# Kernel tuning notes

Measured on AMD Instinct MI355X. Metric: run time of the kernel, lower is better.

The kernel has to match this reference:

```python
import jax, jax.numpy as jnp
import numpy as np

K = 9        # kNN neighbors (ViG default kernel_size=9)
EPS = 1e-5   # BatchNorm eps


def _bn2d(x, gamma, beta):
    # training-mode BatchNorm2d over (B,H,W) per channel; x: [B,C,H,W]
    mean = jnp.mean(x, axis=(0, 2, 3), keepdims=True)
    var = jnp.var(x, axis=(0, 2, 3), keepdims=True)
    g = gamma.reshape(1, -1, 1, 1)
    b = beta.reshape(1, -1, 1, 1)
    return g * (x - mean) * jax.lax.rsqrt(var + EPS) + b


def setup_inputs() -> dict:
    key = jax.random.key(0)
    B, C, H, W = 8, 96, 56, 56
    oup = 192
    ks = jax.random.split(key, 8)
    sc = 0.05
    return {
        "x": jax.random.normal(ks[0], (B, C, H, W), dtype=jnp.float32),
        "W_fc1": jax.random.normal(ks[1], (C, C), dtype=jnp.float32) * sc,
        "b_fc1": jnp.zeros((C,), jnp.float32),
        "g_bn1": jnp.ones((C,), jnp.float32),
        "be_bn1": jnp.zeros((C,), jnp.float32),
        "W_edge": jax.random.normal(ks[2], (2 * C, 2 * C), dtype=jnp.float32) * sc,
        "b_edge": jnp.zeros((2 * C,), jnp.float32),
        "g_bne": jnp.ones((2 * C,), jnp.float32),
        "be_bne": jnp.zeros((2 * C,), jnp.float32),
        "W_fc2": jax.random.normal(ks[3], (2 * C, C), dtype=jnp.float32) * sc,
        "b_fc2": jnp.zeros((C,), jnp.float32),
        "g_bn2": jnp.ones((C,), jnp.float32),
        "be_bn2": jnp.zeros((C,), jnp.float32),
        "g_sabn": jnp.ones((C,), jnp.float32),
        "be_sabn": jnp.zeros((C,), jnp.float32),
        "W_dw": jax.random.normal(ks[4], (oup, C, 3, 3), dtype=jnp.float32) * sc,
        "b_dw": jnp.zeros((oup,), jnp.float32),
        "g_dwbn": jnp.ones((oup,), jnp.float32),
        "be_dwbn": jnp.zeros((oup,), jnp.float32),
    }


def reference(x, W_fc1, b_fc1, g_bn1, be_bn1, W_edge, b_edge, g_bne, be_bne,
              W_fc2, b_fc2, g_bn2, be_bn2, g_sabn, be_sabn,
              W_dw, b_dw, g_dwbn, be_dwbn):
    B, C, H, W = x.shape
    N = H * W
    shortcut = x

    # --- Grapher.fc1: 1x1 conv + BN ---
    y = jnp.einsum('bchw,cd->bdhw', x, W_fc1) + b_fc1[None, :, None, None]
    y = _bn2d(y, g_bn1, be_bn1)

    # --- dynamic kNN graph over flattened tokens ---
    ft = y.reshape(B, C, N).transpose(0, 2, 1)            # [B,N,C]
    sq = jnp.sum(ft * ft, axis=-1)                        # [B,N]
    dist = sq[:, :, None] - 2.0 * jnp.einsum('bnc,bmc->bnm', ft, ft) + sq[:, None, :]
    _, idx = jax.lax.top_k(-dist, K)                      # [B,N,K] nearest neighbors

    # --- EdgeConv: max_k act(BN(W [x_i, x_j - x_i])) ---
    x_j = jnp.take_along_axis(ft[:, :, None, :], idx[..., None], axis=1)  # [B,N,K,C]
    x_i = ft[:, :, None, :]                               # [B,N,1,C]
    e = jnp.concatenate([jnp.broadcast_to(x_i, x_j.shape), x_j - x_i], axis=-1)  # [B,N,K,2C]
    e = jnp.einsum('bnkc,cd->bnkd', e, W_edge) + b_edge
    m = jnp.mean(e, axis=(0, 1, 2))
    v = jnp.var(e, axis=(0, 1, 2))
    e = g_bne * (e - m) * jax.lax.rsqrt(v + EPS) + be_bne
    e = jax.nn.relu(e)
    g = jnp.max(e, axis=2)                                # [B,N,2C] max-aggregation

    # --- Grapher.fc2: 1x1 conv + BN, residual ---
    g = jnp.einsum('bnc,cd->bnd', g, W_fc2) + b_fc2       # [B,N,C]
    g = g.transpose(0, 2, 1).reshape(B, C, H, W)
    g = _bn2d(g, g_bn2, be_bn2)
    y = g + shortcut

    # --- SAEncoder: BN + ReLU ---
    y = jax.nn.relu(_bn2d(y, g_sabn, be_sabn))

    # --- convdw: 3x3 stride-2 conv + BN + ReLU ---
    y = jax.lax.conv_general_dilated(
        y, W_dw, window_strides=(2, 2), padding=((1, 1), (1, 1)),
        dimension_numbers=('NCHW', 'OIHW', 'NCHW')) + b_dw[None, :, None, None]
    y = jax.nn.relu(_bn2d(y, g_dwbn, be_dwbn))
    return y
```

## Files before the change

### kernel.cpp

```cpp
#include <hip/hip_runtime.h>
#include <math.h>

#define B_   8
#define C_   96
#define C2_  192
#define N_   3136
#define R_   25088
#define OUP_ 192
#define HO_  28
#define NO_  784
#define EPS_ 1e-5f
#define QS2  128
#define CAP3 64

typedef short bf16x8 __attribute__((ext_vector_type(8)));
typedef float f32x4  __attribute__((ext_vector_type(4)));

__device__ __forceinline__ int swz16(int i) { return (i & ~15) | ((i & 15) ^ ((i >> 4) & 7)); }

__global__ __launch_bounds__(512) void k_fc1_d(const float* __restrict__ x,
                                               const float* __restrict__ W1,
                                               const float* __restrict__ b1,
                                               double* __restrict__ yd) {
    __shared__ double Wl[96 * 48];
    int tid = threadIdx.x;
    int rl = tid & 255, h = tid >> 8;
    int dbase = blockIdx.y * 48;
    for (int q = tid; q < 96 * 48; q += 512) {
        int c = q / 48, dd = q % 48;
        Wl[c * 48 + dd] = (double)W1[c * 96 + dbase + dd];
    }
    __syncthreads();
    int r = blockIdx.x * 256 + rl;
    int b = r / N_;
    int n = r - b * N_;
    double acc[24];
#pragma unroll
    for (int i = 0; i < 24; i++) acc[i] = 0.0;
    const float* xp = x + (size_t)b * C_ * N_ + n;
    for (int c = 0; c < 96; ++c) {
        double xv = (double)xp[(size_t)c * N_];
        const double* w = &Wl[c * 48 + h * 24];
#pragma unroll
        for (int i = 0; i < 24; ++i) acc[i] += xv * w[i];
    }
    int d0 = dbase + h * 24;
#pragma unroll
    for (int i = 0; i < 24; i++) {
        int d = d0 + i;
        yd[((size_t)b * C_ + d) * N_ + n] = acc[i] + (double)b1[d];
    }
}

__global__ __launch_bounds__(256) void k_stats_chan_d(const double* __restrict__ src,
                                                      double* __restrict__ partial) {
    int c = blockIdx.x;
    int chunk = blockIdx.y;
    const int SPLIT = 16;
    double s = 0.0, ss = 0.0;
    for (int j = chunk * 256 + threadIdx.x; j < R_; j += SPLIT * 256) {
        int b = j / N_, n = j - b * N_;
        double v = src[((size_t)b * C_ + c) * N_ + n];
        s += v;
        ss += v * v;
    }
    __shared__ double red[8];
    for (int off = 32; off; off >>= 1) {
        s += __shfl_down(s, off, 64);
        ss += __shfl_down(ss, off, 64);
    }
    int lane = threadIdx.x & 63, w = threadIdx.x >> 6;
    if (lane == 0) { red[w * 2] = s; red[w * 2 + 1] = ss; }
    __syncthreads();
    if (threadIdx.x == 0) {
        s = red[0] + red[2] + red[4] + red[6];
        ss = red[1] + red[3] + red[5] + red[7];
        partial[(c * SPLIT + chunk) * 2] = s;
        partial[(c * SPLIT + chunk) * 2 + 1] = ss;
    }
}

__global__ void k_stats_reduce_d(const double* __restrict__ partial, double* __restrict__ stats) {
    int c = blockIdx.x * blockDim.x + threadIdx.x;
    if (c >= 96) return;
    double s = 0.0, ss = 0.0;
    for (int k = 0; k < 16; k++) {
        s += partial[(c * 16 + k) * 2];
        ss += partial[(c * 16 + k) * 2 + 1];
    }
    double m = s / (double)R_;
    double var = ss / (double)R_ - m * m;
    stats[c * 2] = m;
    stats[c * 2 + 1] = 1.0 / sqrt(var + 1e-5);
}

__global__ void k_stats_reduce(const float* __restrict__ partial, float* __restrict__ stats,
                               int Cn, int SPLIT, float invcount) {
    int c = blockIdx.x * blockDim.x + threadIdx.x;
    if (c >= Cn) return;
    float s = 0.f, ss = 0.f;
    for (int k = 0; k < SPLIT; k++) {
        s += partial[(c * SPLIT + k) * 2];
        ss += partial[(c * SPLIT + k) * 2 + 1];
    }
    float m = s * invcount;
    float var = ss * invcount - m * m;
    stats[c * 2] = m;
    stats[c * 2 + 1] = 1.0f / sqrtf(var + EPS_);
}

__global__ __launch_bounds__(256) void k_stats_reduce_g(const float* __restrict__ partial,
                                                        float* __restrict__ stats,
                                                        int Cn, int NB, float invcount) {
    int c = blockIdx.x;
    float s = 0.f, ss = 0.f;
    for (int k = threadIdx.x; k < NB; k += 256) {
        s  += partial[(size_t)k * 2 * Cn + c];
        ss += partial[(size_t)k * 2 * Cn + Cn + c];
    }
    __shared__ float red[8];
    for (int off = 32; off; off >>= 1) {
        s += __shfl_down(s, off, 64);
        ss += __shfl_down(ss, off, 64);
    }
    int lane = threadIdx.x & 63, w = threadIdx.x >> 6;
    if (lane == 0) { red[w * 2] = s; red[w * 2 + 1] = ss; }
    __syncthreads();
    if (threadIdx.x == 0) {
        s = red[0] + red[2] + red[4] + red[6];
        ss = red[1] + red[3] + red[5] + red[7];
        float m = s * invcount;
        float var = ss * invcount - m * m;
        stats[c * 2] = m;
        stats[c * 2 + 1] = 1.0f / sqrtf(var + EPS_);
    }
}

__global__ __launch_bounds__(256) void k_bn1_tr(const double* __restrict__ yd,
                                                const double* __restrict__ stats,
                                                const float* __restrict__ g,
                                                const float* __restrict__ be,
                                                float* __restrict__ ftc,
                                                double* __restrict__ ftp64,
                                                unsigned short* __restrict__ fspH,
                                                double* __restrict__ sq64) {
    __shared__ double tile[64 * 97];
    __shared__ double dsq[64][4];
    int b = blockIdx.y;
    int n0 = blockIdx.x * 64;
    int tid = threadIdx.x;
    int n = tid & 63, w = tid >> 6;
    for (int k = 0; k < 24; ++k) {
        int c = k * 4 + w;
        size_t gi = ((size_t)b * C_ + c) * N_ + n0 + n;
        double m = stats[c * 2], rs = stats[c * 2 + 1];
        double v = (double)g[c] * (yd[gi] - m) * rs + (double)be[c];
        ftc[gi] = (float)v;
        tile[n * 97 + c] = v;
    }
    __syncthreads();
    int p = n, q = w;
    double vals[24];
    double s = 0.0;
    const double* lp = &tile[p * 97 + q * 24];
#pragma unroll
    for (int m2 = 0; m2 < 24; ++m2) { vals[m2] = lp[m2]; s += vals[m2] * vals[m2]; }
    dsq[p][q] = s;
    double* dst = ftp64 + ((size_t)b * N_ + n0 + p) * C_ + q * 24;
#pragma unroll
    for (int m2 = 0; m2 < 24; m2 += 2) *(double2*)&dst[m2] = make_double2(vals[m2], vals[m2 + 1]);
    unsigned* hdst = (unsigned*)(fspH + ((size_t)b * N_ + n0 + p) * QS2);
#pragma unroll
    for (int m2 = 0; m2 < 24; m2 += 2) {
        unsigned u0 = __float_as_uint((float)vals[m2]);
        unsigned u1 = __float_as_uint((float)vals[m2 + 1]);
        unsigned h0 = (u0 + 0x7fffu + ((u0 >> 16) & 1u)) >> 16;
        unsigned h1 = (u1 + 0x7fffu + ((u1 >> 16) & 1u)) >> 16;
        hdst[q * 12 + (m2 >> 1)] = h0 | (h1 << 16);
    }
    __syncthreads();
    if (tid < 64) {
        double tot = dsq[tid][0] + dsq[tid][1] + dsq[tid][2] + dsq[tid][3];
        sq64[(size_t)b * N_ + n0 + tid] = tot;
        float t32 = (float)(-0.5 * tot);
        unsigned u0 = __float_as_uint(t32);
        unsigned h0 = (u0 + 0x7fffu + ((u0 >> 16) & 1u)) >> 16;
        float resid = t32 - __uint_as_float(h0 << 16);
        unsigned u1 = __float_as_uint(resid);
        unsigned h1 = (u1 + 0x7fffu + ((u1 >> 16) & 1u)) >> 16;
        unsigned* hd = (unsigned*)(fspH + ((size_t)b * N_ + n0 + tid) * QS2);
        hd[48] = h0 | (h1 << 16);
#pragma unroll
        for (int k2 = 49; k2 < 64; ++k2) hd[k2] = 0u;
    }
}

__global__ __launch_bounds__(256) void k_dist6(const unsigned short* __restrict__ fspH,
                                               unsigned short* __restrict__ poolC,
                                               unsigned* __restrict__ poolCnt) {
    __shared__ __align__(16) char lds[54016];
    float*          cminF = (float*)(lds + 32768);
    unsigned short* poolL = (unsigned short*)(lds + 45312);
    unsigned*       cntL  = (unsigned*)(lds + 53504);
    float*          t9fL  = (float*)(lds + 53760);

    int b = blockIdx.y;
    int q0 = blockIdx.x * 64;
    int tid = threadIdx.x;
    int w = tid >> 6, l = tid & 63;

    {
        const uint4* src = (const uint4*)(fspH + ((size_t)b * N_ + q0) * QS2);
        uint4* dst = (uint4*)lds;
        for (int i = tid; i < 1024; i += 256) dst[swz16(i)] = src[i];
    }
    __syncthreads();
    bf16x8 Bq[4];
    {
        const unsigned short* Ql = (const unsigned short*)lds;
        int qr = w * 16 + (l & 15);
#pragma unroll
        for (int s = 0; s < 3; ++s) {
            int col = (s * 4 + (l >> 4)) ^ (qr & 7);
            Bq[s] = *(const bf16x8*)&Ql[qr * QS2 + col * 8];
        }
        bf16x8 z = {0, 0, 0, 0, 0, 0, 0, 0};
        if ((l >> 4) == 0) { z[0] = (short)0x3F80; z[1] = (short)0x3F80; }
        Bq[3] = z;
    }
    __syncthreads();

    {
        const uint4* src = (const uint4*)(fspH + (size_t)b * N_ * QS2);
        uint4* dst = (uint4*)lds;
        for (int i = tid; i < 1024; i += 256) dst[swz16(i)] = src[i];
    }
    __syncthreads();

    float thr2r = 1e30f;
    int cur = 0;
    for (int t = 0; t < 98; ++t) {
        int ch = (t < 49) ? t : t - 49;
        int c0 = ch * 64;
        bool pf = (t < 97);
        uint4 st0, st1, st2, st3;
        if (pf) {
            int nch = (t + 1 < 49) ? (t + 1) : (t + 1 - 49);
            const uint4* src = (const uint4*)(fspH + ((size_t)b * N_ + nch * 64) * QS2);
            st0 = src[tid]; st1 = src[tid + 256]; st2 = src[tid + 512]; st3 = src[tid + 768];
        }
        const unsigned short* Bc = (const unsigned short*)(lds + cur * 16384);
        f32x4 acc[4];
#pragma unroll
        for (int ct = 0; ct < 4; ++ct) acc[ct] = (f32x4){0.f, 0.f, 0.f, 0.f};
#pragma unroll
        for (int s = 0; s < 4; ++s) {
#pragma unroll
            for (int ct = 0; ct < 4; ++ct) {
                int cr = ct * 16 + (l & 15);
                int col = (s * 4 + (l >> 4)) ^ (cr & 7);
                bf16x8 Ac = *(const bf16x8*)&Bc[cr * QS2 + col * 8];
                acc[ct] = __builtin_amdgcn_mfma_f32_16x16x32_bf16(Ac, Bq[s], acc[ct], 0, 0, 0);
            }
        }
        if (t < 49) {
            float mx = -1e30f;
#pragma unroll
            for (int ct = 0; ct < 4; ++ct)
#pragma unroll
                for (int j = 0; j < 4; ++j) mx = fmaxf(mx, acc[ct][j]);
            mx = fmaxf(mx, __shfl_xor(mx, 16, 64));
            mx = fmaxf(mx, __shfl_xor(mx, 32, 64));
            if (l < 16) cminF[ch * 64 + w * 16 + l] = -2.f * mx;
        } else {
            int qrow = w * 16 + (l & 15);
#pragma unroll
            for (int ct = 0; ct < 4; ++ct)
#pragma unroll
                for (int j = 0; j < 4; ++j) {
                    if (acc[ct][j] >= thr2r) {
                        unsigned pos = atomicAdd(&cntL[qrow], 1u);
                        if (pos < (unsigned)CAP3)
                            poolL[qrow * CAP3 + pos] = (unsigned short)(c0 + ct * 16 + (l >> 4) * 4 + j);
                    }
                }
        }
        if (t == 48) {
            __syncthreads();
            if (tid < 64) {
                float top[9];
#pragma unroll
                for (int j = 0; j < 9; ++j) top[j] = 1e30f;
                for (int q = 0; q < 49; ++q) {
                    float v = cminF[q * 64 + tid];
                    if (v < top[8]) {
                        top[8] = v;
#pragma unroll
                        for (int j = 8; j >= 1; --j)
                            if (top[j] < top[j - 1]) { float tt = top[j]; top[j] = top[j - 1]; top[j - 1] = tt; }
                    }
                }
                float t9 = top[8] + fabsf(top[8]) * 0.008f + 0.75f;
                t9fL[tid] = -0.5f * t9;
                cntL[tid] = 0u;
            }
            __syncthreads();
            thr2r = t9fL[w * 16 + (l & 15)];
        }
        if (pf) {
            uint4* dst = (uint4*)(lds + (cur ^ 1) * 16384);
            dst[swz16(tid)] = st0;
            dst[swz16(tid + 256)] = st1;
            dst[swz16(tid + 512)] = st2;
            dst[swz16(tid + 768)] = st3;
        }
        __syncthreads();
        cur ^= 1;
    }
    if (tid < 64) {
        unsigned c = cntL[tid];
        poolCnt[(size_t)b * N_ + q0 + tid] = (c > (unsigned)CAP3) ? (unsigned)CAP3 : c;
    }
    {
        unsigned* dst = (unsigned*)(poolC + ((size_t)b * N_ + q0) * CAP3);
        const unsigned* src = (const unsigned*)poolL;
        for (int i = tid; i < 64 * CAP3 / 2; i += 256) dst[i] = src[i];
    }
}

__global__ __launch_bounds__(256) void k_rerank_d(const unsigned short* __restrict__ poolC,
                                                  const unsigned* __restrict__ poolCnt,
                                                  const double* __restrict__ ftp64,
                                                  const double* __restrict__ sq64,
                                                  int* __restrict__ idx) {
    int tid = threadIdx.x;
    int wv = tid >> 6, l = tid & 63;
    int rr = blockIdx.x * 4 + wv;
    int b = rr / N_;
    int cnt = (int)poolCnt[rr];
    if (cnt > CAP3) cnt = CAP3;
    int e = l & 3;
    double qreg[24];
    {
        const double* qb = ftp64 + (size_t)rr * C_ + e * 24;
#pragma unroll
        for (int m = 0; m < 24; ++m) qreg[m] = qb[m];
    }
    double dv[4];
    int jv[4];
#pragma unroll
    for (int gG = 0; gG < 4; ++gG) { dv[gG] = 1e300; jv[gG] = 0x7fffffff; }
#pragma unroll
    for (int gG = 0; gG < 4; ++gG) {
        if (gG * 16 >= cnt) break;
        int ci = gG * 16 + (l >> 2);
        bool valid = ci < cnt;
        int j = valid ? (int)poolC[(size_t)rr * CAP3 + ci] : 0;
        const double* cb = ftp64 + ((size_t)b * N_ + j) * C_ + e * 24;
        double p = 0.0;
#pragma unroll
        for (int m = 0; m < 24; ++m) p += qreg[m] * cb[m];
        p += __shfl_xor(p, 1, 64);
        p += __shfl_xor(p, 2, 64);
        if (valid) {
            dv[gG] = sq64[(size_t)b * N_ + j] - 2.0 * p;
            jv[gG] = j;
        }
    }
#pragma unroll
    for (int r = 0; r < 9; ++r) {
        double dm = dv[0]; int jm = jv[0];
#pragma unroll
        for (int gG = 1; gG < 4; ++gG)
            if (dv[gG] < dm || (dv[gG] == dm && jv[gG] < jm)) { dm = dv[gG]; jm = jv[gG]; }
#pragma unroll
        for (int off = 1; off <= 32; off <<= 1) {
            double od = __shfl_xor(dm, off, 64);
            int oj = __shfl_xor(jm, off, 64);
            if (od < dm || (od == dm && oj < jm)) { dm = od; jm = oj; }
        }
        if (l == 0) idx[(size_t)rr * 9 + r] = jm;
#pragma unroll
        for (int gG = 0; gG < 4; ++gG)
            if (jv[gG] == jm) dv[gG] = 1e300;
    }
}

__global__ __launch_bounds__(512) void k_gemm_uv2(const float* __restrict__ ftc,
                                                  const float* __restrict__ We,
                                                  const float* __restrict__ beb,
                                                  float* __restrict__ u,
                                                  float* __restrict__ v) {
    __shared__ float Wl[2][96 * 48];
    int tid = threadIdx.x;
    int rl = tid & 255, h = tid >> 8;
    int dbase = blockIdx.y * 48;
    for (int q = tid; q < 96 * 48; q += 512) {
        int c = q / 48, dd = q % 48;
        float wb = We[(96 + c) * C2_ + dbase + dd];
        Wl[1][q] = wb;
        Wl[0][q] = We[c * C2_ + dbase + dd] - wb;
    }
    __syncthreads();
    int r = blockIdx.x * 256 + rl;
    int b = r / N_, n = r - b * N_;
    float a0[24], a1[24];
#pragma unroll
    for (int i = 0; i < 24; i++) { a0[i] = 0.f; a1[i] = 0.f; }
    const float* xp = ftc + (size_t)b * C_ * N_ + n;
    for (int c = 0; c < 96; ++c) {
        float xv = xp[(size_t)c * N_];
        const float4* w40 = (const float4*)&Wl[0][c * 48 + h * 24];
        const float4* w41 = (const float4*)&Wl[1][c * 48 + h * 24];
#pragma unroll
        for (int i = 0; i < 6; ++i) {
            float4 w0 = w40[i], w1 = w41[i];
            a0[i * 4 + 0] += xv * w0.x; a0[i * 4 + 1] += xv * w0.y;
            a0[i * 4 + 2] += xv * w0.z; a0[i * 4 + 3] += xv * w0.w;
            a1[i * 4 + 0] += xv * w1.x; a1[i * 4 + 1] += xv * w1.y;
            a1[i * 4 + 2] += xv * w1.z; a1[i * 4 + 3] += xv * w1.w;
        }
    }
    int d0 = dbase + h * 24;
    float* up = u + (size_t)r * C2_ + d0;
    float* vp = v + (size_t)r * C2_ + d0;
#pragma unroll
    for (int i = 0; i < 6; ++i) {
        float4 ou, ov;
        ou.x = a0[i * 4 + 0] + beb[d0 + i * 4 + 0];
        ou.y = a0[i * 4 + 1] + beb[d0 + i * 4 + 1];
        ou.z = a0[i * 4 + 2] + beb[d0 + i * 4 + 2];
        ou.w = a0[i * 4 + 3] + beb[d0 + i * 4 + 3];
        ov.x = a1[i * 4 + 0]; ov.y = a1[i * 4 + 1];
        ov.z = a1[i * 4 + 2]; ov.w = a1[i * 4 + 3];
        ((float4*)up)[i] = ou;
        ((float4*)vp)[i] = ov;
    }
}

__global__ __launch_bounds__(192) void k_bne_stats(const float* __restrict__ u,
                                                   const float* __restrict__ v,
                                                   const int* __restrict__ idx,
                                                   float* __restrict__ partial) {
    int d = threadIdx.x;
    int row0 = blockIdx.x * 32;
    int b = row0 / N_;
    float s = 0.f, ss = 0.f;
    for (int r = 0; r < 32; ++r) {
        int row = row0 + r;
        float ud = u[(size_t)row * C2_ + d];
        const int* ip = idx + (size_t)row * 9;
#pragma unroll
        for (int k = 0; k < 9; k++) {
            int j = ip[k];
            float e = ud + v[((size_t)b * N_ + j) * C2_ + d];
            s += e;
            ss += e * e;
        }
    }
    partial[(size_t)blockIdx.x * 384 + d] = s;
    partial[(size_t)blockIdx.x * 384 + 192 + d] = ss;
}

__global__ __launch_bounds__(192) void k_edge_fc2_st(const float* __restrict__ u,
                                                     const float* __restrict__ v,
                                                     const int* __restrict__ idx,
                                                     const float* __restrict__ statsE,
                                                     const float* __restrict__ ge,
                                                     const float* __restrict__ bee,
                                                     const float* __restrict__ W2,
                                                     const float* __restrict__ b2,
                                                     float* __restrict__ out2,
                                                     float* __restrict__ partialE) {
    __shared__ float gl[16][C2_];
    __shared__ float g2[C_][16];
    int tid = threadIdx.x;
    int row0 = blockIdx.x * 16;
    int b = row0 / N_;
    int n0 = row0 - b * N_;
    {
        int d = tid;
        float m = statsE[d * 2], rs = statsE[d * 2 + 1];
        float ga = ge[d], bb = bee[d];
        for (int r = 0; r < 16; ++r) {
            int row = row0 + r;
            float ud = u[(size_t)row * C2_ + d];
            const int* ip = idx + (size_t)row * 9;
            float gm = 0.f;
#pragma unroll
            for (int k = 0; k < 9; k++) {
                int j = ip[k];
                float e = ud + v[((size_t)b * N_ + j) * C2_ + d];
                float val = ga * (e - m) * rs + bb;
                gm = fmaxf(gm, val);
            }
            gl[r][d] = gm;
        }
    }
    __syncthreads();
    {
        int rr = tid / 24;
        int dq = tid % 24;
        for (int rep = 0; rep < 2; ++rep) {
            int r = rr + rep * 8;
            float4 acc = *(const float4*)&b2[dq * 4];
            for (int d = 0; d < C2_; ++d) {
                float gv = gl[r][d];
                float4 w = *(const float4*)&W2[d * C_ + dq * 4];
                acc.x += gv * w.x;
                acc.y += gv * w.y;
                acc.z += gv * w.z;
                acc.w += gv * w.w;
            }
            g2[dq * 4 + 0][r] = acc.x;
            g2[dq * 4 + 1][r] = acc.y;
            g2[dq * 4 + 2][r] = acc.z;
            g2[dq * 4 + 3][r] = acc.w;
        }
    }
    __syncthreads();
    for (int q = tid; q < 96 * 4; q += 192) {
        int dd = q / 4, part = q % 4;
        float4 val = *(const float4*)&g2[dd][part * 4];
        *(float4*)&out2[((size_t)b * C_ + dd) * N_ + n0 + part * 4] = val;
    }
    {
        int c = tid >> 1, h = tid & 1;
        float s = 0.f, ss = 0.f;
#pragma unroll
        for (int r = 0; r < 8; ++r) {
            float vv = g2[c][h * 8 + r];
            s += vv;
            ss += vv * vv;
        }
        s += __shfl_xor(s, 1, 64);
        ss += __shfl_xor(ss, 1, 64);
        if (h == 0) {
            partialE[(size_t)blockIdx.x * 192 + c] = s;
            partialE[(size_t)blockIdx.x * 192 + 96 + c] = ss;
        }
    }
}

__global__ __launch_bounds__(256) void k_bn2_add_st(const float* __restrict__ out2,
                                                    const float* __restrict__ x,
                                                    const float* __restrict__ stats,
                                                    const float* __restrict__ g,
                                                    const float* __restrict__ be,
                                                    float* __restrict__ t,
                                                    float* __restrict__ partial) {
    int c = blockIdx.x;
    int chunk = blockIdx.y;
    const int SPLIT = 16;
    float m = stats[c * 2], rs = stats[c * 2 + 1];
    float ga = g[c], bb = be[c];
    float s = 0.f, ss = 0.f;
    for (int j = chunk * 256 + threadIdx.x; j < R_; j += SPLIT * 256) {
        int b = j / N_, n = j - b * N_;
        size_t i = ((size_t)b * C_ + c) * N_ + n;
        float tv = ga * (out2[i] - m) * rs + bb + x[i];
        t[i] = tv;
        s += tv;
        ss += tv * tv;
    }
    __shared__ float red[8];
    for (int off = 32; off; off >>= 1) {
        s += __shfl_down(s, off, 64);
        ss += __shfl_down(ss, off, 64);
    }
    int lane = threadIdx.x & 63, w = threadIdx.x >> 6;
    if (lane == 0) { red[w * 2] = s; red[w * 2 + 1] = ss; }
    __syncthreads();
    if (threadIdx.x == 0) {
        s = red[0] + red[2] + red[4] + red[6];
        ss = red[1] + red[3] + red[5] + red[7];
        partial[(c * SPLIT + chunk) * 2] = s;
        partial[(c * SPLIT + chunk) * 2 + 1] = ss;
    }
}

__global__ __launch_bounds__(256) void k_wtr(const float* __restrict__ Wd, float* __restrict__ Wt) {
    int i = blockIdx.x * 256 + threadIdx.x;
    if (i >= 192 * 864) return;
    int oc = i / 864, k = i % 864;
    Wt[(size_t)k * 192 + oc] = Wd[i];
}

__global__ __launch_bounds__(256) void k_conv16n(const float* __restrict__ t,
                                                 const float* __restrict__ statsS,
                                                 const float* __restrict__ gS,
                                                 const float* __restrict__ beS,
                                                 const float* __restrict__ Wt,
                                                 const float* __restrict__ bd,
                                                 float* __restrict__ z,
                                                 float* __restrict__ partialD) {
    __shared__ float redc[4][32];
    int b = blockIdx.z;
    int oc0 = blockIdx.y * 16;
    int p = blockIdx.x * 256 + threadIdx.x;
    bool valid = p < NO_;
    int oh = valid ? p / HO_ : 0, ow = valid ? p % HO_ : 0;
    float acc[16];
#pragma unroll
    for (int i = 0; i < 16; i++) acc[i] = 0.f;
    int ih0 = oh * 2 - 1, iw0 = ow * 2 - 1;
    const float* tb = t + (size_t)b * C_ * N_;
    for (int ic = 0; ic < 96; ++ic) {
        float m = statsS[ic * 2], rs = statsS[ic * 2 + 1], ga = gS[ic];
        float sc_ = ga * rs;
        float sh_ = beS[ic] - ga * m * rs;
        const float* sp = tb + (size_t)ic * N_;
        float in[9];
#pragma unroll
        for (int kh = 0; kh < 3; kh++) {
            int ih = ih0 + kh;
            bool okh = valid && ((unsigned)ih < 56u);
#pragma unroll
            for (int kw = 0; kw < 3; kw++) {
                int iw = iw0 + kw;
                bool ok = okh && ((unsigned)iw < 56u);
                float raw = ok ? sp[ih * 56 + iw] : 0.f;
                in[kh * 3 + kw] = ok ? fmaxf(sc_ * raw + sh_, 0.f) : 0.f;
            }
        }
        const float* wk = Wt + (size_t)(ic * 9) * 192 + oc0;
#pragma unroll
        for (int q = 0; q < 9; q++) {
            float iv = in[q];
            const float4* w4 = (const float4*)&wk[q * 192];
#pragma unroll
            for (int j = 0; j < 4; j++) {
                float4 w = w4[j];
                acc[j * 4 + 0] += iv * w.x;
                acc[j * 4 + 1] += iv * w.y;
                acc[j * 4 + 2] += iv * w.z;
                acc[j * 4 + 3] += iv * w.w;
            }
        }
    }
    float s8[16];
#pragma unroll
    for (int i = 0; i < 16; i++) {
        float ov = acc[i] + bd[oc0 + i];
        if (valid) z[((size_t)b * OUP_ + oc0 + i) * NO_ + p] = ov;
        s8[i] = valid ? ov : 0.f;
    }
    int w = threadIdx.x >> 6;
#pragma unroll
    for (int i = 0; i < 16; ++i) {
        float s = s8[i], ss = s8[i] * s8[i];
        for (int off = 32; off; off >>= 1) {
            s += __shfl_down(s, off, 64);
            ss += __shfl_down(ss, off, 64);
        }
        if ((threadIdx.x & 63) == 0) { redc[w][i * 2] = s; redc[w][i * 2 + 1] = ss; }
    }
    __syncthreads();
    if (threadIdx.x < 32) {
        float v = redc[0][threadIdx.x] + redc[1][threadIdx.x] + redc[2][threadIdx.x] + redc[3][threadIdx.x];
        int blk = (b * 12 + blockIdx.y) * 4 + blockIdx.x;
        partialD[blk * 32 + threadIdx.x] = v;
    }
}

__global__ void k_stats_reduce_conv(const float* __restrict__ partialD, float* __restrict__ stats) {
    int c = threadIdx.x;
    if (c >= 192) return;
    int y = c >> 4, o = c & 15;
    float s = 0.f, ss = 0.f;
    for (int bb = 0; bb < 8; ++bb)
        for (int x2 = 0; x2 < 4; ++x2) {
            int blk = (bb * 12 + y) * 4 + x2;
            s += partialD[blk * 32 + o * 2];
            ss += partialD[blk * 32 + o * 2 + 1];
        }
    float m = s / 6272.f;
    float var = ss / 6272.f - m * m;
    stats[c * 2] = m;
    stats[c * 2 + 1] = 1.0f / sqrtf(var + EPS_);
}

__global__ __launch_bounds__(256) void k_out(const float* __restrict__ z,
                                             const float* __restrict__ stats,
                                             const float* __restrict__ g,
                                             const float* __restrict__ be,
                                             float* __restrict__ out) {
    int i = blockIdx.x * 256 + threadIdx.x;
    if (i >= B_ * OUP_ * NO_) return;
    int c = (i / NO_) % OUP_;
    out[i] = fmaxf(g[c] * (z[i] - stats[c * 2]) * stats[c * 2 + 1] + be[c], 0.f);
}

extern "C" void kernel_launch(void* const* d_in, const int* in_sizes, int n_in,
                              void* d_out, int out_size, void* d_ws, size_t ws_size,
                              hipStream_t stream) {
    const float* x     = (const float*)d_in[0];
    const float* W_fc1 = (const float*)d_in[1];
    const float* b_fc1 = (const float*)d_in[2];
    const float* g_bn1 = (const float*)d_in[3];
    const float* be_bn1= (const float*)d_in[4];
    const float* W_edge= (const float*)d_in[5];
    const float* b_edge= (const float*)d_in[6];
    const float* g_bne = (const float*)d_in[7];
    const float* be_bne= (const float*)d_in[8];
    const float* W_fc2 = (const float*)d_in[9];
    const float* b_fc2 = (const float*)d_in[10];
    const float* g_bn2 = (const float*)d_in[11];
    const float* be_bn2= (const float*)d_in[12];
    const float* g_sabn= (const float*)d_in[13];
    const float* be_sabn=(const float*)d_in[14];
    const float* W_dw  = (const float*)d_in[15];
    const float* b_dw  = (const float*)d_in[16];
    const float* g_dwbn= (const float*)d_in[17];
    const float* be_dwbn=(const float*)d_in[18];

    char* base = (char*)d_ws;
    float*  ftc   = (float*)(base + 0);
    double* ftp64 = (double*)(base + 9633792);
    float*  uu    = (float*)(base + 9633792);
    double* yd    = (double*)(base + 28901376);
    float*  vv    = (float*)(base + 28901376);
    unsigned short* fspH = (unsigned short*)(base + 48168960);
    float*  out2  = (float*)(base + 48168960);
    unsigned short* poolC = (unsigned short*)(base + 57802752);
    float*  tbuf  = (float*)(base + 57802752);
    double* sq64  = (double*)(base + 67436544);
    int*    idx   = (int*)(base + 67637248);
    unsigned* poolCnt = (unsigned*)(base + 68540416);
    float*  partial = (float*)(base + 68741120);
    double* partiald = (double*)(base + 68741120);
    double* stats1d = (double*)(base + 69945344);
    float*  statsE  = (float*)(base + 69946880);
    float*  stats2  = (float*)(base + 69948416);
    float*  statsS  = (float*)(base + 69949952);
    float*  statsD  = (float*)(base + 69951488);
    float*  zbuf  = (float*)(base + 69953024);
    float*  Wt    = (float*)(base + 74769920);

    k_wtr<<<648, 256, 0, stream>>>(W_dw, Wt);

    k_fc1_d<<<dim3(98, 2), 512, 0, stream>>>(x, W_fc1, b_fc1, yd);
    k_stats_chan_d<<<dim3(96, 16), 256, 0, stream>>>(yd, partiald);
    k_stats_reduce_d<<<1, 256, 0, stream>>>(partiald, stats1d);
    k_bn1_tr<<<dim3(49, B_), 256, 0, stream>>>(yd, stats1d, g_bn1, be_bn1, ftc, ftp64, fspH, sq64);

    k_dist6<<<dim3(49, B_), 256, 0, stream>>>(fspH, poolC, poolCnt);
    k_rerank_d<<<6272, 256, 0, stream>>>(poolC, poolCnt, ftp64, sq64, idx);

    k_gemm_uv2<<<dim3(98, 4), 512, 0, stream>>>(ftc, W_edge, b_edge, uu, vv);

    k_bne_stats<<<784, 192, 0, stream>>>(uu, vv, idx, partial);
    k_stats_reduce_g<<<192, 256, 0, stream>>>(partial, statsE, 192, 784, 1.0f / 225792.0f);
    k_edge_fc2_st<<<1568, 192, 0, stream>>>(uu, vv, idx, statsE, g_bne, be_bne, W_fc2, b_fc2, out2, partial);
    k_stats_reduce_g<<<96, 256, 0, stream>>>(partial, stats2, 96, 1568, 1.0f / (float)R_);

    k_bn2_add_st<<<dim3(96, 16), 256, 0, stream>>>(out2, x, stats2, g_bn2, be_bn2, tbuf, partial);
    k_stats_reduce<<<1, 256, 0, stream>>>(partial, statsS, 96, 16, 1.0f / (float)R_);

    k_conv16n<<<dim3(4, 12, 8), 256, 0, stream>>>(tbuf, statsS, g_sabn, be_sabn, Wt, b_dw, zbuf, partial);
    k_stats_reduce_conv<<<1, 192, 0, stream>>>(partial, statsD);
    k_out<<<4705, 256, 0, stream>>>(zbuf, statsD, g_dwbn, be_dwbn, (float*)d_out);
}
```

Before: 685.9 us.

## Split conv input channels across blocks, stage weights in LDS, combine partials separately

```diff
diff --git a/kernel.cpp b/kernel.cpp
--- a/kernel.cpp
+++ b/kernel.cpp
@@ -579,42 +579,46 @@
     }
 }
 
-__global__ __launch_bounds__(256) void k_wtr(const float* __restrict__ Wd, float* __restrict__ Wt) {
-    int i = blockIdx.x * 256 + threadIdx.x;
-    if (i >= 192 * 864) return;
-    int oc = i / 864, k = i % 864;
-    Wt[(size_t)k * 192 + oc] = Wd[i];
-}
-
-__global__ __launch_bounds__(256) void k_conv16n(const float* __restrict__ t,
+__global__ __launch_bounds__(256) void k_conv_ic(const float* __restrict__ t,
                                                  const float* __restrict__ statsS,
                                                  const float* __restrict__ gS,
                                                  const float* __restrict__ beS,
-                                                 const float* __restrict__ Wt,
-                                                 const float* __restrict__ bd,
-                                                 float* __restrict__ z,
-                                                 float* __restrict__ partialD) {
-    __shared__ float redc[4][32];
+                                                 const float* __restrict__ Wd,
+                                                 float* __restrict__ zp) {
+    __shared__ float Wl[48 * 9 * 16];
+    __shared__ float scl[48], shf[48];
     int b = blockIdx.z;
-    int oc0 = blockIdx.y * 16;
+    int yy = blockIdx.y;
+    int oc0 = (yy >> 1) * 16;
+    int half = yy & 1;
+    int icb = half * 48;
     int p = blockIdx.x * 256 + threadIdx.x;
-    bool valid = p < NO_;
-    int oh = valid ? p / HO_ : 0, ow = valid ? p % HO_ : 0;
+    for (int i = threadIdx.x; i < 48 * 9 * 16; i += 256) {
+        int oc = i & 15, icq = i >> 4;
+        Wl[i] = Wd[(size_t)(oc0 + oc) * 864 + icb * 9 + icq];
+    }
+    if (threadIdx.x < 48) {
+        int c = icb + threadIdx.x;
+        float m = statsS[c * 2], rs = statsS[c * 2 + 1], ga = gS[c];
+        scl[threadIdx.x] = ga * rs;
+        shf[threadIdx.x] = beS[c] - ga * m * rs;
+    }
+    __syncthreads();
+    if (p >= NO_) return;
+    int oh = p / HO_, ow = p % HO_;
     float acc[16];
 #pragma unroll
     for (int i = 0; i < 16; i++) acc[i] = 0.f;
     int ih0 = oh * 2 - 1, iw0 = ow * 2 - 1;
-    const float* tb = t + (size_t)b * C_ * N_;
-    for (int ic = 0; ic < 96; ++ic) {
-        float m = statsS[ic * 2], rs = statsS[ic * 2 + 1], ga = gS[ic];
-        float sc_ = ga * rs;
-        float sh_ = beS[ic] - ga * m * rs;
+    const float* tb = t + (size_t)b * C_ * N_ + (size_t)icb * N_;
+    for (int ic = 0; ic < 48; ++ic) {
         const float* sp = tb + (size_t)ic * N_;
+        float sc_ = scl[ic], sh_ = shf[ic];
         float in[9];
 #pragma unroll
         for (int kh = 0; kh < 3; kh++) {
             int ih = ih0 + kh;
-            bool okh = valid && ((unsigned)ih < 56u);
+            bool okh = (unsigned)ih < 56u;
 #pragma unroll
             for (int kw = 0; kw < 3; kw++) {
                 int iw = iw0 + kw;
@@ -623,11 +627,10 @@
                 in[kh * 3 + kw] = ok ? fmaxf(sc_ * raw + sh_, 0.f) : 0.f;
             }
         }
-        const float* wk = Wt + (size_t)(ic * 9) * 192 + oc0;
 #pragma unroll
         for (int q = 0; q < 9; q++) {
             float iv = in[q];
-            const float4* w4 = (const float4*)&wk[q * 192];
+            const float4* w4 = (const float4*)&Wl[(ic * 9 + q) * 16];
 #pragma unroll
             for (int j = 0; j < 4; j++) {
                 float4 w = w4[j];
@@ -638,46 +641,42 @@
             }
         }
     }
-    float s8[16];
-#pragma unroll
-    for (int i = 0; i < 16; i++) {
-        float ov = acc[i] + bd[oc0 + i];
-        if (valid) z[((size_t)b * OUP_ + oc0 + i) * NO_ + p] = ov;
-        s8[i] = valid ? ov : 0.f;
-    }
-    int w = threadIdx.x >> 6;
-#pragma unroll
-    for (int i = 0; i < 16; ++i) {
-        float s = s8[i], ss = s8[i] * s8[i];
-        for (int off = 32; off; off >>= 1) {
-            s += __shfl_down(s, off, 64);
-            ss += __shfl_down(ss, off, 64);
-        }
-        if ((threadIdx.x & 63) == 0) { redc[w][i * 2] = s; redc[w][i * 2 + 1] = ss; }
-    }
-    __syncthreads();
-    if (threadIdx.x < 32) {
-        float v = redc[0][threadIdx.x] + redc[1][threadIdx.x] + redc[2][threadIdx.x] + redc[3][threadIdx.x];
-        int blk = (b * 12 + blockIdx.y) * 4 + blockIdx.x;
-        partialD[blk * 32 + threadIdx.x] = v;
-    }
-}
-
-__global__ void k_stats_reduce_conv(const float* __restrict__ partialD, float* __restrict__ stats) {
-    int c = threadIdx.x;
-    if (c >= 192) return;
-    int y = c >> 4, o = c & 15;
+#pragma unroll
+    for (int i = 0; i < 16; i++)
+        zp[((size_t)(half * B_ + b) * OUP_ + oc0 + i) * NO_ + p] = acc[i];
+}
+
+__global__ __launch_bounds__(256) void k_zcomb(const float* __restrict__ zp,
+                                               const float* __restrict__ bd,
+                                               float* __restrict__ z,
+                                               float* __restrict__ partial) {
+    int c = blockIdx.x;
+    int chunk = blockIdx.y;
+    const int SPLIT = 8;
+    float bias = bd[c];
     float s = 0.f, ss = 0.f;
-    for (int bb = 0; bb < 8; ++bb)
-        for (int x2 = 0; x2 < 4; ++x2) {
-            int blk = (bb * 12 + y) * 4 + x2;
-            s += partialD[blk * 32 + o * 2];
-            ss += partialD[blk * 32 + o * 2 + 1];
-        }
-    float m = s / 6272.f;
-    float var = ss / 6272.f - m * m;
-    stats[c * 2] = m;
-    stats[c * 2 + 1] = 1.0f / sqrtf(var + EPS_);
+    for (int j = chunk * 256 + threadIdx.x; j < B_ * NO_; j += SPLIT * 256) {
+        int b = j / NO_, p = j - b * NO_;
+        size_t i = ((size_t)b * OUP_ + c) * NO_ + p;
+        float v = zp[i] + zp[((size_t)(B_ + b) * OUP_ + c) * NO_ + p] + bias;
+        z[i] = v;
+        s += v;
+        ss += v * v;
+    }
+    __shared__ float red[8];
+    for (int off = 32; off; off >>= 1) {
+        s += __shfl_down(s, off, 64);
+        ss += __shfl_down(ss, off, 64);
+    }
+    int lane = threadIdx.x & 63, w = threadIdx.x >> 6;
+    if (lane == 0) { red[w * 2] = s; red[w * 2 + 1] = ss; }
+    __syncthreads();
+    if (threadIdx.x == 0) {
+        s = red[0] + red[2] + red[4] + red[6];
+        ss = red[1] + red[3] + red[5] + red[7];
+        partial[(c * SPLIT + chunk) * 2] = s;
+        partial[(c * SPLIT + chunk) * 2 + 1] = ss;
+    }
 }
 
 __global__ __launch_bounds__(256) void k_out(const float* __restrict__ z,
@@ -716,6 +715,7 @@
 
     char* base = (char*)d_ws;
     float*  ftc   = (float*)(base + 0);
+    float*  zp    = (float*)(base + 0);
     double* ftp64 = (double*)(base + 9633792);
     float*  uu    = (float*)(base + 9633792);
     double* yd    = (double*)(base + 28901376);
@@ -735,9 +735,6 @@
     float*  statsS  = (float*)(base + 69949952);
     float*  statsD  = (float*)(base + 69951488);
     float*  zbuf  = (float*)(base + 69953024);
-    float*  Wt    = (float*)(base + 74769920);
-
-    k_wtr<<<648, 256, 0, stream>>>(W_dw, Wt);
 
     k_fc1_d<<<dim3(98, 2), 512, 0, stream>>>(x, W_fc1, b_fc1, yd);
     k_stats_chan_d<<<dim3(96, 16), 256, 0, stream>>>(yd, partiald);
@@ -757,7 +754,8 @@
     k_bn2_add_st<<<dim3(96, 16), 256, 0, stream>>>(out2, x, stats2, g_bn2, be_bn2, tbuf, partial);
     k_stats_reduce<<<1, 256, 0, stream>>>(partial, statsS, 96, 16, 1.0f / (float)R_);
 
-    k_conv16n<<<dim3(4, 12, 8), 256, 0, stream>>>(tbuf, statsS, g_sabn, be_sabn, Wt, b_dw, zbuf, partial);
-    k_stats_reduce_conv<<<1, 192, 0, stream>>>(partial, statsD);
+    k_conv_ic<<<dim3(4, 24, 8), 256, 0, stream>>>(tbuf, statsS, g_sabn, be_sabn, W_dw, zp);
+    k_zcomb<<<dim3(192, 8), 256, 0, stream>>>(zp, b_dw, zbuf, partial);
+    k_stats_reduce<<<1, 256, 0, stream>>>(partial, statsD, 192, 8, 1.0f / 6272.0f);
     k_out<<<4705, 256, 0, stream>>>(zbuf, statsD, g_dwbn, be_dwbn, (float*)d_out);
 }
```

After: 587.7 us. -14.3%, faster.
